# Optimization experiments

Measured on AMD Instinct MI355X. Metric: run time of the kernel, lower is better.

The kernel has to match this reference:

```python
import jax, jax.numpy as jnp
import numpy as np

N_NODES = 100000
N_HEDGES = 20000
N_PAIRS = 1600000
D = 128


def setup_inputs() -> dict:
    key = jax.random.key(0)
    k1, k2, k3, k4, k5 = jax.random.split(key, 5)
    features = jax.random.normal(k1, (N_NODES, D), dtype=jnp.float32)
    W = jax.random.normal(k2, (D, D), dtype=jnp.float32) * (1.0 / np.sqrt(D))
    b = jax.random.normal(k3, (D,), dtype=jnp.float32) * 0.01
    node_idx = jax.random.randint(k4, (N_PAIRS,), 0, N_NODES, dtype=jnp.int32)
    hedge_idx = jax.random.randint(k5, (N_PAIRS,), 0, N_HEDGES, dtype=jnp.int32)
    return {"features": features, "W": W, "b": b,
            "node_idx": node_idx, "hedge_idx": hedge_idx, "n_hedges": N_HEDGES}


def reference(features, W, b, node_idx, hedge_idx, n_hedges):
    # features: [N, D]; (node_idx, hedge_idx): [E] incidence pairs
    N = features.shape[0]
    ones = jnp.ones(node_idx.shape, dtype=features.dtype)
    # node -> hyperedge mean (DGL copy_u + mean over 'in' etype)
    deg_e = jax.ops.segment_sum(ones, hedge_idx, num_segments=n_hedges)  # [He]
    h_edge = jax.ops.segment_sum(features[node_idx], hedge_idx, num_segments=n_hedges)
    h_edge = h_edge / jnp.maximum(deg_e, 1.0)[:, None]  # zero-degree edges -> 0
    # hyperedge -> node mean (copy_u + mean over 'contains' etype)
    deg_n = jax.ops.segment_sum(ones, node_idx, num_segments=N)  # [N]
    h_node = jax.ops.segment_sum(h_edge[hedge_idx], node_idx, num_segments=N)
    h_node = h_node / jnp.maximum(deg_n, 1.0)[:, None]
    # nn.Linear: x @ W.T + b
    return h_node @ W.T + b
```

## Files before the change

kernel.cpp:

```cpp
#include <hip/hip_runtime.h>

static constexpr int kD = 128;
static constexpr int kHedges = 20000;

static constexpr int kNCE = 157;
static constexpr int kCapCE = 11264;
static constexpr int kNCN = 196;
static constexpr int kCapCN = 9216;
static constexpr int kSliceE4 = 1664;
static constexpr int kSliceN4 = 1408;
static constexpr int kPmax = 3200;

__device__ __forceinline__ float u2f(unsigned u) { return __uint_as_float(u); }
__device__ __forceinline__ unsigned f2u(float f) { return __float_as_uint(f); }

__device__ __forceinline__ unsigned bfpack(float x, float y) {
  unsigned ux = f2u(x); ux = (ux + 0x7FFFu + ((ux >> 16) & 1u)) >> 16;
  unsigned uy = f2u(y); uy = (uy + 0x7FFFu + ((uy >> 16) & 1u)) & 0xFFFF0000u;
  return ux | uy;
}
__device__ __forceinline__ void bf8_acc(uint4 v, float* a) {
  a[0] += u2f(v.x << 16); a[1] += u2f(v.x & 0xFFFF0000u);
  a[2] += u2f(v.y << 16); a[3] += u2f(v.y & 0xFFFF0000u);
  a[4] += u2f(v.z << 16); a[5] += u2f(v.z & 0xFFFF0000u);
  a[6] += u2f(v.w << 16); a[7] += u2f(v.w & 0xFFFF0000u);
}

__global__ __launch_bounds__(256) void partition_coarse(
    const float* __restrict__ feat, unsigned* __restrict__ feat_bf, int n_feat,
    const int* __restrict__ node_idx, const int* __restrict__ hedge_idx,
    int n_pairs,
    int* __restrict__ gcnt_e, int* __restrict__ buf_e,
    int* __restrict__ gcnt_n, int* __restrict__ buf_n) {
  __shared__ unsigned lbuf_e[kPmax];
  __shared__ unsigned lbuf_n[kPmax];
  __shared__ int he[kNCE], se[kNCE];
  __shared__ int hn[kNCN], sn_[kNCN];
  __shared__ int wtot[4];
  const int tid = threadIdx.x;
  {
    const int n8 = n_feat >> 3;
    for (int t = blockIdx.x * 256 + tid; t < n8; t += gridDim.x * 256) {
      long long i = (long long)t * 8;
      const float4 v0 = *(const float4*)(feat + i);
      const float4 v1 = *(const float4*)(feat + i + 4);
      uint4 o;
      o.x = bfpack(v0.x, v0.y); o.y = bfpack(v0.z, v0.w);
      o.z = bfpack(v1.x, v1.y); o.w = bfpack(v1.z, v1.w);
      *(uint4*)(feat_bf + (i >> 1)) = o;
    }
  }
  const int per_block = (n_pairs + gridDim.x - 1) / gridDim.x;
  const int s = blockIdx.x * per_block;
  const int e = min(s + per_block, n_pairs);
  const int cnt = max(e - s, 0);
  for (int i = tid; i < kNCE; i += 256) he[i] = 0;
  for (int i = tid; i < kNCN; i += 256) hn[i] = 0;
  __syncthreads();
  for (int i = s + tid; i < e; i += 256) {
    atomicAdd(&he[hedge_idx[i] >> 7], 1);
    atomicAdd(&hn[node_idx[i] >> 9], 1);
  }
  __syncthreads();
  const int lane = tid & 63, wid = tid >> 6;
  {
    int v = (tid < kNCE) ? he[tid] : 0;
    int x = v;
#pragma unroll
    for (int d = 1; d < 64; d <<= 1) {
      int y = __shfl_up(x, d, 64);
      if (lane >= d) x += y;
    }
    if (lane == 63) wtot[wid] = x;
    __syncthreads();
    int add = 0;
    for (int w = 0; w < wid; ++w) add += wtot[w];
    if (tid < kNCE) {
      int lofs = x + add - v;
      int base = (v > 0) ? atomicAdd(&gcnt_e[tid], v) : 0;
      se[tid] = base - lofs;
      he[tid] = lofs;
    }
  }
  __syncthreads();
  {
    int v = (tid < kNCN) ? hn[tid] : 0;
    int x = v;
#pragma unroll
    for (int d = 1; d < 64; d <<= 1) {
      int y = __shfl_up(x, d, 64);
      if (lane >= d) x += y;
    }
    if (lane == 63) wtot[wid] = x;
    __syncthreads();
    int add = 0;
    for (int w = 0; w < wid; ++w) add += wtot[w];
    if (tid < kNCN) {
      int lofs = x + add - v;
      int base = (v > 0) ? atomicAdd(&gcnt_n[tid], v) : 0;
      sn_[tid] = base - lofs;
      hn[tid] = lofs;
    }
  }
  __syncthreads();
  for (int i = s + tid; i < e; i += 256) {
    const unsigned n = (unsigned)node_idx[i];
    const unsigned h = (unsigned)hedge_idx[i];
    const int be = (int)(h >> 7);
    const int p = atomicAdd(&he[be], 1);
    lbuf_e[p] = (n << 15) | h;
    const int bn = (int)(n >> 9);
    const int q = atomicAdd(&hn[bn], 1);
    lbuf_n[q] = (h << 17) | n;
  }
  __syncthreads();
  for (int i = tid; i < cnt; i += 256) {
    const unsigned v = lbuf_e[i];
    const int h = (int)(v & 0x7FFFu);
    const int n = (int)(v >> 15);
    const int b = h >> 7;
    const int pe = se[b] + i;
    if (pe < kCapCE) buf_e[(long long)b * kCapCE + pe] = (n << 7) | (h & 127);
  }
  for (int i = tid; i < cnt; i += 256) {
    const unsigned v = lbuf_n[i];
    const int n = (int)(v & 0x1FFFFu);
    const int h = (int)(v >> 17);
    const int b = n >> 9;
    const int pn = sn_[b] + i;
    if (pn < kCapCN) buf_n[(long long)b * kCapCN + pn] = (h << 9) | (n & 511);
  }
}

__global__ __launch_bounds__(512) void subsort_kernel(
    int* __restrict__ buf_e, const int* __restrict__ gcnt_e, int* __restrict__ seg_e,
    int* __restrict__ buf_n, const int* __restrict__ gcnt_n, int* __restrict__ seg_n) {
  __shared__ int sbuf[kCapCE];
  __shared__ int bins[513];
  __shared__ int cur[512];
  __shared__ int segs[513];
  __shared__ int wtot[8];
  const int tid = threadIdx.x;
  int nbins, shift, cnt; int* src; int* segout;
  if (blockIdx.x < kNCE) {
    int cb = blockIdx.x; nbins = 128; shift = 7;
    src = buf_e + (long long)cb * kCapCE;
    cnt = min(gcnt_e[cb], kCapCE);
    segout = seg_e + cb * 129;
  } else {
    int cb = blockIdx.x - kNCE; nbins = 512; shift = 9;
    src = buf_n + (long long)cb * kCapCN;
    cnt = min(gcnt_n[cb], kCapCN);
    segout = seg_n + cb * 513;
  }
  const int mask = nbins - 1;
  for (int i = tid; i < nbins; i += 512) bins[i] = 0;
  __syncthreads();
  for (int i = tid; i < cnt; i += 512) atomicAdd(&bins[src[i] & mask], 1);
  __syncthreads();
  const int lane = tid & 63, wid = tid >> 6;
  int v = (tid < nbins) ? bins[tid] : 0;
  int x = v;
#pragma unroll
  for (int d = 1; d < 64; d <<= 1) {
    int y = __shfl_up(x, d, 64);
    if (lane >= d) x += y;
  }
  if (lane == 63) wtot[wid] = x;
  __syncthreads();
  int add = 0;
  for (int w = 0; w < wid; ++w) add += wtot[w];
  if (tid < nbins) { segs[tid + 1] = x + add; cur[tid] = x + add - v; }
  if (tid == 0) segs[0] = 0;
  __syncthreads();
  for (int i = tid; i < cnt; i += 512) {
    int p = src[i];
    int r = atomicAdd(&cur[p & mask], 1);
    sbuf[r] = p >> shift;
  }
  __syncthreads();
  for (int i = tid; i < cnt; i += 512) src[i] = sbuf[i];
  for (int j = tid; j <= nbins; j += 512) segout[j] = segs[j];
}

__global__ __launch_bounds__(256) void gather_edge_v4(
    const unsigned* __restrict__ feat_bf, const int* __restrict__ buf_e,
    const int* __restrict__ seg_e, unsigned* __restrict__ h_edge, int n_hedges) {
  __shared__ int ebuf[kSliceE4];
  __shared__ int segl[17];
  const int b = blockIdx.x;
  const int tid = threadIdx.x;
  const int h0 = b * 16;
  const int cb = h0 >> 7, j0 = h0 & 127;
  if (tid < 17) segl[tid] = seg_e[cb * 129 + j0 + tid];
  __syncthreads();
  const int sbase = segl[0];
  const int n_sl = min(segl[16] - sbase, kSliceE4);
  const int* src = buf_e + (long long)cb * kCapCE + sbase;
  for (int i = tid; i < n_sl; i += 256) ebuf[i] = src[i];
  __syncthreads();
  const int g = tid >> 4, lane = tid & 15, cw = lane * 4;
  int gh = h0 + g;
  if (gh >= n_hedges) return;
  const int deg = segl[g + 1] - segl[g];
  const int s0 = min(segl[g] - sbase, n_sl);
  const int e0 = min(segl[g + 1] - sbase, n_sl);
  float a[8] = {}, a2[8] = {};
  int j = s0;
  const int jend8 = s0 + ((e0 - s0) & ~7);
  if (j < jend8) {
    uint4 A0 = *(const uint4*)(feat_bf + (long long)ebuf[j] * 64 + cw);
    uint4 A1 = *(const uint4*)(feat_bf + (long long)ebuf[j + 1] * 64 + cw);
    uint4 A2 = *(const uint4*)(feat_bf + (long long)ebuf[j + 2] * 64 + cw);
    uint4 A3 = *(const uint4*)(feat_bf + (long long)ebuf[j + 3] * 64 + cw);
    uint4 A4 = *(const uint4*)(feat_bf + (long long)ebuf[j + 4] * 64 + cw);
    uint4 A5 = *(const uint4*)(feat_bf + (long long)ebuf[j + 5] * 64 + cw);
    uint4 A6 = *(const uint4*)(feat_bf + (long long)ebuf[j + 6] * 64 + cw);
    uint4 A7 = *(const uint4*)(feat_bf + (long long)ebuf[j + 7] * 64 + cw);
    j += 8;
    for (; j < jend8; j += 8) {
      uint4 B0 = *(const uint4*)(feat_bf + (long long)ebuf[j] * 64 + cw);
      uint4 B1 = *(const uint4*)(feat_bf + (long long)ebuf[j + 1] * 64 + cw);
      uint4 B2 = *(const uint4*)(feat_bf + (long long)ebuf[j + 2] * 64 + cw);
      uint4 B3 = *(const uint4*)(feat_bf + (long long)ebuf[j + 3] * 64 + cw);
      uint4 B4 = *(const uint4*)(feat_bf + (long long)ebuf[j + 4] * 64 + cw);
      uint4 B5 = *(const uint4*)(feat_bf + (long long)ebuf[j + 5] * 64 + cw);
      uint4 B6 = *(const uint4*)(feat_bf + (long long)ebuf[j + 6] * 64 + cw);
      uint4 B7 = *(const uint4*)(feat_bf + (long long)ebuf[j + 7] * 64 + cw);
      bf8_acc(A0, a); bf8_acc(A1, a2); bf8_acc(A2, a); bf8_acc(A3, a2);
      bf8_acc(A4, a); bf8_acc(A5, a2); bf8_acc(A6, a); bf8_acc(A7, a2);
      A0 = B0; A1 = B1; A2 = B2; A3 = B3;
      A4 = B4; A5 = B5; A6 = B6; A7 = B7;
    }
    bf8_acc(A0, a); bf8_acc(A1, a2); bf8_acc(A2, a); bf8_acc(A3, a2);
    bf8_acc(A4, a); bf8_acc(A5, a2); bf8_acc(A6, a); bf8_acc(A7, a2);
  }
  for (; j < e0; ++j) {
    uint4 v = *(const uint4*)(feat_bf + (long long)ebuf[j] * 64 + cw);
    bf8_acc(v, a);
  }
#pragma unroll
  for (int t = 0; t < 8; ++t) a[t] += a2[t];
  float inv = 1.0f / fmaxf((float)deg, 1.0f);
  uint4 o;
  o.x = bfpack(a[0] * inv, a[1] * inv);
  o.y = bfpack(a[2] * inv, a[3] * inv);
  o.z = bfpack(a[4] * inv, a[5] * inv);
  o.w = bfpack(a[6] * inv, a[7] * inv);
  *(uint4*)(h_edge + (long long)gh * 64 + cw) = o;
}

static constexpr int kWRow = 68;
__global__ __launch_bounds__(256) void edge_linear_v4(
    unsigned* __restrict__ h_edge, const float* __restrict__ W, int n_rows) {
  __shared__ unsigned Wt2[kD * kWRow];
  __shared__ float hT[kD * 64];
  const int tid = threadIdx.x;
  const int row0 = blockIdx.x * 64;
  for (int i = tid; i < kD * 64; i += 256) {
    int k = i & 127, j = i >> 7;
    float c0 = W[(2 * j) * kD + k];
    float c1 = W[(2 * j + 1) * kD + k];
    Wt2[k * kWRow + j] = bfpack(c0, c1);
  }
  {
    const int r = tid & 63, o = tid >> 6;
    const uint4* hp = (const uint4*)(h_edge + (long long)(row0 + r) * 64 + o * 16);
#pragma unroll
    for (int q = 0; q < 4; ++q) {
      uint4 v = hp[q];
      int k0 = o * 32 + q * 8;
      hT[(k0 + 0) * 64 + r] = u2f(v.x << 16);
      hT[(k0 + 1) * 64 + r] = u2f(v.x & 0xFFFF0000u);
      hT[(k0 + 2) * 64 + r] = u2f(v.y << 16);
      hT[(k0 + 3) * 64 + r] = u2f(v.y & 0xFFFF0000u);
      hT[(k0 + 4) * 64 + r] = u2f(v.z << 16);
      hT[(k0 + 5) * 64 + r] = u2f(v.z & 0xFFFF0000u);
      hT[(k0 + 6) * 64 + r] = u2f(v.w << 16);
      hT[(k0 + 7) * 64 + r] = u2f(v.w & 0xFFFF0000u);
    }
  }
  __syncthreads();
  const int c8 = tid & 15;
  const int rg = tid >> 4;
  float4 acc[4][2] = {};
#pragma unroll 2
  for (int k = 0; k < kD; ++k) {
    const uint4 wp = *(const uint4*)(&Wt2[k * kWRow + c8 * 4]);
    const float4 h4 = *(const float4*)(&hT[k * 64 + rg * 4]);
    const float w0 = u2f(wp.x << 16), w1 = u2f(wp.x & 0xFFFF0000u);
    const float w2 = u2f(wp.y << 16), w3 = u2f(wp.y & 0xFFFF0000u);
    const float w4 = u2f(wp.z << 16), w5 = u2f(wp.z & 0xFFFF0000u);
    const float w6 = u2f(wp.w << 16), w7 = u2f(wp.w & 0xFFFF0000u);
    const float hh[4] = {h4.x, h4.y, h4.z, h4.w};
#pragma unroll
    for (int i = 0; i < 4; ++i) {
      acc[i][0].x = fmaf(hh[i], w0, acc[i][0].x);
      acc[i][0].y = fmaf(hh[i], w1, acc[i][0].y);
      acc[i][0].z = fmaf(hh[i], w2, acc[i][0].z);
      acc[i][0].w = fmaf(hh[i], w3, acc[i][0].w);
      acc[i][1].x = fmaf(hh[i], w4, acc[i][1].x);
      acc[i][1].y = fmaf(hh[i], w5, acc[i][1].y);
      acc[i][1].z = fmaf(hh[i], w6, acc[i][1].z);
      acc[i][1].w = fmaf(hh[i], w7, acc[i][1].w);
    }
  }
  long long rr = row0 + rg * 4;
#pragma unroll
  for (int i = 0; i < 4; ++i) {
    uint4 o;
    o.x = bfpack(acc[i][0].x, acc[i][0].y);
    o.y = bfpack(acc[i][0].z, acc[i][0].w);
    o.z = bfpack(acc[i][1].x, acc[i][1].y);
    o.w = bfpack(acc[i][1].z, acc[i][1].w);
    *(uint4*)(h_edge + (rr + i) * 64 + c8 * 4) = o;
  }
}

__global__ __launch_bounds__(256) void gather_node_v4(
    const unsigned* __restrict__ t_edge, const int* __restrict__ buf_n,
    const int* __restrict__ seg_n, const float* __restrict__ bias,
    float* __restrict__ out, int n_nodes) {
  __shared__ int ebuf[kSliceN4];
  __shared__ int segl[65];
  const int b = blockIdx.x;
  const int tid = threadIdx.x;
  const int n0 = b * 64;
  const int cb = n0 >> 9, j0 = n0 & 511;
  if (tid < 65) segl[tid] = seg_n[cb * 513 + j0 + tid];
  __syncthreads();
  const int sbase = segl[0];
  const int n_sl = min(segl[64] - sbase, kSliceN4);
  const int* src = buf_n + (long long)cb * kCapCN + sbase;
  for (int i = tid; i < n_sl; i += 256) ebuf[i] = src[i];
  __syncthreads();
  const int g = tid >> 4, lane = tid & 15, cw = lane * 4;
  const float4 b0 = *(const float4*)(bias + lane * 8);
  const float4 b1 = *(const float4*)(bias + lane * 8 + 4);
  for (int nl = g; nl < 64; nl += 16) {
    int gn = n0 + nl;
    if (gn >= n_nodes) continue;
    const int deg = segl[nl + 1] - segl[nl];
    const int s0 = min(segl[nl] - sbase, n_sl);
    const int e0 = min(segl[nl + 1] - sbase, n_sl);
    float a[8] = {}, a2[8] = {};
    int j = s0;
    const int jend8 = s0 + ((e0 - s0) & ~7);
    if (j < jend8) {
      uint4 A0 = *(const uint4*)(t_edge + (long long)ebuf[j] * 64 + cw);
      uint4 A1 = *(const uint4*)(t_edge + (long long)ebuf[j + 1] * 64 + cw);
      uint4 A2 = *(const uint4*)(t_edge + (long long)ebuf[j + 2] * 64 + cw);
      uint4 A3 = *(const uint4*)(t_edge + (long long)ebuf[j + 3] * 64 + cw);
      uint4 A4 = *(const uint4*)(t_edge + (long long)ebuf[j + 4] * 64 + cw);
      uint4 A5 = *(const uint4*)(t_edge + (long long)ebuf[j + 5] * 64 + cw);
      uint4 A6 = *(const uint4*)(t_edge + (long long)ebuf[j + 6] * 64 + cw);
      uint4 A7 = *(const uint4*)(t_edge + (long long)ebuf[j + 7] * 64 + cw);
      j += 8;
      for (; j < jend8; j += 8) {
        uint4 B0 = *(const uint4*)(t_edge + (long long)ebuf[j] * 64 + cw);
        uint4 B1 = *(const uint4*)(t_edge + (long long)ebuf[j + 1] * 64 + cw);
        uint4 B2 = *(const uint4*)(t_edge + (long long)ebuf[j + 2] * 64 + cw);
        uint4 B3 = *(const uint4*)(t_edge + (long long)ebuf[j + 3] * 64 + cw);
        uint4 B4 = *(const uint4*)(t_edge + (long long)ebuf[j + 4] * 64 + cw);
        uint4 B5 = *(const uint4*)(t_edge + (long long)ebuf[j + 5] * 64 + cw);
        uint4 B6 = *(const uint4*)(t_edge + (long long)ebuf[j + 6] * 64 + cw);
        uint4 B7 = *(const uint4*)(t_edge + (long long)ebuf[j + 7] * 64 + cw);
        bf8_acc(A0, a); bf8_acc(A1, a2); bf8_acc(A2, a); bf8_acc(A3, a2);
        bf8_acc(A4, a); bf8_acc(A5, a2); bf8_acc(A6, a); bf8_acc(A7, a2);
        A0 = B0; A1 = B1; A2 = B2; A3 = B3;
        A4 = B4; A5 = B5; A6 = B6; A7 = B7;
      }
      bf8_acc(A0, a); bf8_acc(A1, a2); bf8_acc(A2, a); bf8_acc(A3, a2);
      bf8_acc(A4, a); bf8_acc(A5, a2); bf8_acc(A6, a); bf8_acc(A7, a2);
    }
    for (; j < e0; ++j) {
      uint4 v = *(const uint4*)(t_edge + (long long)ebuf[j] * 64 + cw);
      bf8_acc(v, a);
    }
#pragma unroll
    for (int t = 0; t < 8; ++t) a[t] += a2[t];
    float inv = 1.0f / fmaxf((float)deg, 1.0f);
    float4 o0, o1;
    o0.x = fmaf(a[0], inv, b0.x); o0.y = fmaf(a[1], inv, b0.y);
    o0.z = fmaf(a[2], inv, b0.z); o0.w = fmaf(a[3], inv, b0.w);
    o1.x = fmaf(a[4], inv, b1.x); o1.y = fmaf(a[5], inv, b1.y);
    o1.z = fmaf(a[6], inv, b1.z); o1.w = fmaf(a[7], inv, b1.w);
    float* op = out + (long long)gn * kD + lane * 8;
    *(float4*)op = o0;
    *(float4*)(op + 4) = o1;
  }
}

extern "C" void kernel_launch(void* const* d_in, const int* in_sizes, int n_in,
                              void* d_out, int out_size, void* d_ws, size_t ws_size,
                              hipStream_t stream) {
  const float* feat      = (const float*)d_in[0];
  const float* W         = (const float*)d_in[1];
  const float* b         = (const float*)d_in[2];
  const int*   node_idx  = (const int*)d_in[3];
  const int*   hedge_idx = (const int*)d_in[4];

  const int n_pairs  = in_sizes[3];
  const int n_nodes  = in_sizes[0] / kD;
  const int n_hedges = kHedges;
  const int n_feat   = in_sizes[0];

  unsigned* feat_bf = (unsigned*)d_out;

  const int n_rows_pad = ((n_hedges + 63) / 64) * 64;
  unsigned* h_edge = (unsigned*)d_ws;
  int* buf_e = (int*)(h_edge + (size_t)n_rows_pad * 64);
  int* buf_n = buf_e + (size_t)kNCE * kCapCE;
  int* seg_e = buf_n + (size_t)kNCN * kCapCN;
  int* seg_n = seg_e + (size_t)kNCE * 129;
  int* gcnt_e = seg_n + (size_t)kNCN * 513;
  int* gcnt_n = gcnt_e + kNCE;

  hipMemsetAsync(gcnt_e, 0, (size_t)(kNCE + kNCN) * sizeof(int), stream);

  int pgrid = (n_pairs + kPmax - 1) / kPmax;
  if (pgrid < 512) pgrid = 512;

  partition_coarse<<<pgrid, 256, 0, stream>>>(
      feat, feat_bf, n_feat,
      node_idx, hedge_idx, n_pairs, gcnt_e, buf_e, gcnt_n, buf_n);

  subsort_kernel<<<kNCE + kNCN, 512, 0, stream>>>(
      buf_e, gcnt_e, seg_e, buf_n, gcnt_n, seg_n);

  gather_edge_v4<<<(n_hedges + 15) / 16, 256, 0, stream>>>(
      feat_bf, buf_e, seg_e, h_edge, n_hedges);

  edge_linear_v4<<<n_rows_pad / 64, 256, 0, stream>>>(h_edge, W, n_rows_pad);

  gather_node_v4<<<(n_nodes + 63) / 64, 256, 0, stream>>>(
      h_edge, buf_n, seg_n, b, (float*)d_out, n_nodes);
}
```

Baseline: 278.9 us.

## Fuse edge linear transform into edge gather and widen subsort blocks

Merges the hyperedge mean-gather and the per-edge linear projection into one kernel. Each block keeps its 16 averaged rows in shared memory and multiplies them by a bf16 copy of W, so the intermediate h_edge round trip and one launch go away. The cost is that every one of the 1250 blocks now rebuilds the transposed W in shared memory, which adds about 34KB of LDS per block and could cut occupancy in the gather phase. Separately, the subsort kernel now runs with 1024 threads per block instead of 512.

```diff
diff --git a/kernel.cpp b/kernel.cpp
--- a/kernel.cpp
+++ b/kernel.cpp
@@ -10,6 +10,7 @@
 static constexpr int kSliceE4 = 1664;
 static constexpr int kSliceN4 = 1408;
 static constexpr int kPmax = 3200;
+static constexpr int kWRow = 68;
 
 __device__ __forceinline__ float u2f(unsigned u) { return __uint_as_float(u); }
 __device__ __forceinline__ unsigned f2u(float f) { return __float_as_uint(f); }
@@ -132,14 +133,14 @@
   }
 }
 
-__global__ __launch_bounds__(512) void subsort_kernel(
+__global__ __launch_bounds__(1024) void subsort_kernel(
     int* __restrict__ buf_e, const int* __restrict__ gcnt_e, int* __restrict__ seg_e,
     int* __restrict__ buf_n, const int* __restrict__ gcnt_n, int* __restrict__ seg_n) {
   __shared__ int sbuf[kCapCE];
   __shared__ int bins[513];
   __shared__ int cur[512];
   __shared__ int segs[513];
-  __shared__ int wtot[8];
+  __shared__ int wtot[16];
   const int tid = threadIdx.x;
   int nbins, shift, cnt; int* src; int* segout;
   if (blockIdx.x < kNCE) {
@@ -154,9 +155,9 @@
     segout = seg_n + cb * 513;
   }
   const int mask = nbins - 1;
-  for (int i = tid; i < nbins; i += 512) bins[i] = 0;
-  __syncthreads();
-  for (int i = tid; i < cnt; i += 512) atomicAdd(&bins[src[i] & mask], 1);
+  for (int i = tid; i < nbins; i += 1024) bins[i] = 0;
+  __syncthreads();
+  for (int i = tid; i < cnt; i += 1024) atomicAdd(&bins[src[i] & mask], 1);
   __syncthreads();
   const int lane = tid & 63, wid = tid >> 6;
   int v = (tid < nbins) ? bins[tid] : 0;
@@ -173,147 +174,115 @@
   if (tid < nbins) { segs[tid + 1] = x + add; cur[tid] = x + add - v; }
   if (tid == 0) segs[0] = 0;
   __syncthreads();
-  for (int i = tid; i < cnt; i += 512) {
+  for (int i = tid; i < cnt; i += 1024) {
     int p = src[i];
     int r = atomicAdd(&cur[p & mask], 1);
     sbuf[r] = p >> shift;
   }
   __syncthreads();
-  for (int i = tid; i < cnt; i += 512) src[i] = sbuf[i];
-  for (int j = tid; j <= nbins; j += 512) segout[j] = segs[j];
-}
-
-__global__ __launch_bounds__(256) void gather_edge_v4(
+  for (int i = tid; i < cnt; i += 1024) src[i] = sbuf[i];
+  for (int j = tid; j <= nbins; j += 1024) segout[j] = segs[j];
+}
+
+__global__ __launch_bounds__(256) void gather_edge_fused(
     const unsigned* __restrict__ feat_bf, const int* __restrict__ buf_e,
-    const int* __restrict__ seg_e, unsigned* __restrict__ h_edge, int n_hedges) {
+    const int* __restrict__ seg_e, const float* __restrict__ W,
+    unsigned* __restrict__ t_edge, int n_hedges) {
   __shared__ int ebuf[kSliceE4];
   __shared__ int segl[17];
+  __shared__ unsigned Wt2[kD * kWRow];
+  __shared__ float hrow[16][132];
   const int b = blockIdx.x;
   const int tid = threadIdx.x;
   const int h0 = b * 16;
   const int cb = h0 >> 7, j0 = h0 & 127;
   if (tid < 17) segl[tid] = seg_e[cb * 129 + j0 + tid];
-  __syncthreads();
-  const int sbase = segl[0];
-  const int n_sl = min(segl[16] - sbase, kSliceE4);
-  const int* src = buf_e + (long long)cb * kCapCE + sbase;
-  for (int i = tid; i < n_sl; i += 256) ebuf[i] = src[i];
-  __syncthreads();
-  const int g = tid >> 4, lane = tid & 15, cw = lane * 4;
-  int gh = h0 + g;
-  if (gh >= n_hedges) return;
-  const int deg = segl[g + 1] - segl[g];
-  const int s0 = min(segl[g] - sbase, n_sl);
-  const int e0 = min(segl[g + 1] - sbase, n_sl);
-  float a[8] = {}, a2[8] = {};
-  int j = s0;
-  const int jend8 = s0 + ((e0 - s0) & ~7);
-  if (j < jend8) {
-    uint4 A0 = *(const uint4*)(feat_bf + (long long)ebuf[j] * 64 + cw);
-    uint4 A1 = *(const uint4*)(feat_bf + (long long)ebuf[j + 1] * 64 + cw);
-    uint4 A2 = *(const uint4*)(feat_bf + (long long)ebuf[j + 2] * 64 + cw);
-    uint4 A3 = *(const uint4*)(feat_bf + (long long)ebuf[j + 3] * 64 + cw);
-    uint4 A4 = *(const uint4*)(feat_bf + (long long)ebuf[j + 4] * 64 + cw);
-    uint4 A5 = *(const uint4*)(feat_bf + (long long)ebuf[j + 5] * 64 + cw);
-    uint4 A6 = *(const uint4*)(feat_bf + (long long)ebuf[j + 6] * 64 + cw);
-    uint4 A7 = *(const uint4*)(feat_bf + (long long)ebuf[j + 7] * 64 + cw);
-    j += 8;
-    for (; j < jend8; j += 8) {
-      uint4 B0 = *(const uint4*)(feat_bf + (long long)ebuf[j] * 64 + cw);
-      uint4 B1 = *(const uint4*)(feat_bf + (long long)ebuf[j + 1] * 64 + cw);
-      uint4 B2 = *(const uint4*)(feat_bf + (long long)ebuf[j + 2] * 64 + cw);
-      uint4 B3 = *(const uint4*)(feat_bf + (long long)ebuf[j + 3] * 64 + cw);
-      uint4 B4 = *(const uint4*)(feat_bf + (long long)ebuf[j + 4] * 64 + cw);
-      uint4 B5 = *(const uint4*)(feat_bf + (long long)ebuf[j + 5] * 64 + cw);
-      uint4 B6 = *(const uint4*)(feat_bf + (long long)ebuf[j + 6] * 64 + cw);
-      uint4 B7 = *(const uint4*)(feat_bf + (long long)ebuf[j + 7] * 64 + cw);
-      bf8_acc(A0, a); bf8_acc(A1, a2); bf8_acc(A2, a); bf8_acc(A3, a2);
-      bf8_acc(A4, a); bf8_acc(A5, a2); bf8_acc(A6, a); bf8_acc(A7, a2);
-      A0 = B0; A1 = B1; A2 = B2; A3 = B3;
-      A4 = B4; A5 = B5; A6 = B6; A7 = B7;
-    }
-    bf8_acc(A0, a); bf8_acc(A1, a2); bf8_acc(A2, a); bf8_acc(A3, a2);
-    bf8_acc(A4, a); bf8_acc(A5, a2); bf8_acc(A6, a); bf8_acc(A7, a2);
-  }
-  for (; j < e0; ++j) {
-    uint4 v = *(const uint4*)(feat_bf + (long long)ebuf[j] * 64 + cw);
-    bf8_acc(v, a);
-  }
-#pragma unroll
-  for (int t = 0; t < 8; ++t) a[t] += a2[t];
-  float inv = 1.0f / fmaxf((float)deg, 1.0f);
-  uint4 o;
-  o.x = bfpack(a[0] * inv, a[1] * inv);
-  o.y = bfpack(a[2] * inv, a[3] * inv);
-  o.z = bfpack(a[4] * inv, a[5] * inv);
-  o.w = bfpack(a[6] * inv, a[7] * inv);
-  *(uint4*)(h_edge + (long long)gh * 64 + cw) = o;
-}
-
-static constexpr int kWRow = 68;
-__global__ __launch_bounds__(256) void edge_linear_v4(
-    unsigned* __restrict__ h_edge, const float* __restrict__ W, int n_rows) {
-  __shared__ unsigned Wt2[kD * kWRow];
-  __shared__ float hT[kD * 64];
-  const int tid = threadIdx.x;
-  const int row0 = blockIdx.x * 64;
   for (int i = tid; i < kD * 64; i += 256) {
     int k = i & 127, j = i >> 7;
     float c0 = W[(2 * j) * kD + k];
     float c1 = W[(2 * j + 1) * kD + k];
     Wt2[k * kWRow + j] = bfpack(c0, c1);
   }
+  __syncthreads();
+  const int sbase = segl[0];
+  const int n_sl = min(segl[16] - sbase, kSliceE4);
+  const int* src = buf_e + (long long)cb * kCapCE + sbase;
+  for (int i = tid; i < n_sl; i += 256) ebuf[i] = src[i];
+  __syncthreads();
+  const int g = tid >> 4, lane = tid & 15, cw = lane * 4;
+  const int gh = h0 + g;
+  float a[8] = {}, a2[8] = {};
+  int deg = 0;
+  if (gh < n_hedges) {
+    deg = segl[g + 1] - segl[g];
+    const int s0 = min(segl[g] - sbase, n_sl);
+    const int e0 = min(segl[g + 1] - sbase, n_sl);
+    int j = s0;
+    const int jend8 = s0 + ((e0 - s0) & ~7);
+    if (j < jend8) {
+      uint4 A0 = *(const uint4*)(feat_bf + (long long)ebuf[j] * 64 + cw);
+      uint4 A1 = *(const uint4*)(feat_bf + (long long)ebuf[j + 1] * 64 + cw);
+      uint4 A2 = *(const uint4*)(feat_bf + (long long)ebuf[j + 2] * 64 + cw);
+      uint4 A3 = *(const uint4*)(feat_bf + (long long)ebuf[j + 3] * 64 + cw);
+      uint4 A4 = *(const uint4*)(feat_bf + (long long)ebuf[j + 4] * 64 + cw);
+      uint4 A5 = *(const uint4*)(feat_bf + (long long)ebuf[j + 5] * 64 + cw);
+      uint4 A6 = *(const uint4*)(feat_bf + (long long)ebuf[j + 6] * 64 + cw);
+      uint4 A7 = *(const uint4*)(feat_bf + (long long)ebuf[j + 7] * 64 + cw);
+      j += 8;
+      for (; j < jend8; j += 8) {
+        uint4 B0 = *(const uint4*)(feat_bf + (long long)ebuf[j] * 64 + cw);
+        uint4 B1 = *(const uint4*)(feat_bf + (long long)ebuf[j + 1] * 64 + cw);
+        uint4 B2 = *(const uint4*)(feat_bf + (long long)ebuf[j + 2] * 64 + cw);
+        uint4 B3 = *(const uint4*)(feat_bf + (long long)ebuf[j + 3] * 64 + cw);
+        uint4 B4 = *(const uint4*)(feat_bf + (long long)ebuf[j + 4] * 64 + cw);
+        uint4 B5 = *(const uint4*)(feat_bf + (long long)ebuf[j + 5] * 64 + cw);
+        uint4 B6 = *(const uint4*)(feat_bf + (long long)ebuf[j + 6] * 64 + cw);
+        uint4 B7 = *(const uint4*)(feat_bf + (long long)ebuf[j + 7] * 64 + cw);
+        bf8_acc(A0, a); bf8_acc(A1, a2); bf8_acc(A2, a); bf8_acc(A3, a2);
+        bf8_acc(A4, a); bf8_acc(A5, a2); bf8_acc(A6, a); bf8_acc(A7, a2);
+        A0 = B0; A1 = B1; A2 = B2; A3 = B3;
+        A4 = B4; A5 = B5; A6 = B6; A7 = B7;
+      }
+      bf8_acc(A0, a); bf8_acc(A1, a2); bf8_acc(A2, a); bf8_acc(A3, a2);
+      bf8_acc(A4, a); bf8_acc(A5, a2); bf8_acc(A6, a); bf8_acc(A7, a2);
+    }
+    for (; j < e0; ++j) {
+      uint4 v = *(const uint4*)(feat_bf + (long long)ebuf[j] * 64 + cw);
+      bf8_acc(v, a);
+    }
+  }
   {
-    const int r = tid & 63, o = tid >> 6;
-    const uint4* hp = (const uint4*)(h_edge + (long long)(row0 + r) * 64 + o * 16);
-#pragma unroll
-    for (int q = 0; q < 4; ++q) {
-      uint4 v = hp[q];
-      int k0 = o * 32 + q * 8;
-      hT[(k0 + 0) * 64 + r] = u2f(v.x << 16);
-      hT[(k0 + 1) * 64 + r] = u2f(v.x & 0xFFFF0000u);
-      hT[(k0 + 2) * 64 + r] = u2f(v.y << 16);
-      hT[(k0 + 3) * 64 + r] = u2f(v.y & 0xFFFF0000u);
-      hT[(k0 + 4) * 64 + r] = u2f(v.z << 16);
-      hT[(k0 + 5) * 64 + r] = u2f(v.z & 0xFFFF0000u);
-      hT[(k0 + 6) * 64 + r] = u2f(v.w << 16);
-      hT[(k0 + 7) * 64 + r] = u2f(v.w & 0xFFFF0000u);
-    }
-  }
-  __syncthreads();
-  const int c8 = tid & 15;
-  const int rg = tid >> 4;
-  float4 acc[4][2] = {};
+    const float inv = 1.0f / fmaxf((float)deg, 1.0f);
+    float4 r0, r1;
+    r0.x = (a[0] + a2[0]) * inv; r0.y = (a[1] + a2[1]) * inv;
+    r0.z = (a[2] + a2[2]) * inv; r0.w = (a[3] + a2[3]) * inv;
+    r1.x = (a[4] + a2[4]) * inv; r1.y = (a[5] + a2[5]) * inv;
+    r1.z = (a[6] + a2[6]) * inv; r1.w = (a[7] + a2[7]) * inv;
+    *(float4*)(&hrow[g][lane * 8]) = r0;
+    *(float4*)(&hrow[g][lane * 8 + 4]) = r1;
+  }
+  __syncthreads();
+  float acc[8] = {};
 #pragma unroll 2
   for (int k = 0; k < kD; ++k) {
-    const uint4 wp = *(const uint4*)(&Wt2[k * kWRow + c8 * 4]);
-    const float4 h4 = *(const float4*)(&hT[k * 64 + rg * 4]);
-    const float w0 = u2f(wp.x << 16), w1 = u2f(wp.x & 0xFFFF0000u);
-    const float w2 = u2f(wp.y << 16), w3 = u2f(wp.y & 0xFFFF0000u);
-    const float w4 = u2f(wp.z << 16), w5 = u2f(wp.z & 0xFFFF0000u);
-    const float w6 = u2f(wp.w << 16), w7 = u2f(wp.w & 0xFFFF0000u);
-    const float hh[4] = {h4.x, h4.y, h4.z, h4.w};
-#pragma unroll
-    for (int i = 0; i < 4; ++i) {
-      acc[i][0].x = fmaf(hh[i], w0, acc[i][0].x);
-      acc[i][0].y = fmaf(hh[i], w1, acc[i][0].y);
-      acc[i][0].z = fmaf(hh[i], w2, acc[i][0].z);
-      acc[i][0].w = fmaf(hh[i], w3, acc[i][0].w);
-      acc[i][1].x = fmaf(hh[i], w4, acc[i][1].x);
-      acc[i][1].y = fmaf(hh[i], w5, acc[i][1].y);
-      acc[i][1].z = fmaf(hh[i], w6, acc[i][1].z);
-      acc[i][1].w = fmaf(hh[i], w7, acc[i][1].w);
-    }
-  }
-  long long rr = row0 + rg * 4;
-#pragma unroll
-  for (int i = 0; i < 4; ++i) {
+    const uint4 wp = *(const uint4*)(&Wt2[k * kWRow + lane * 4]);
+    const float hk = hrow[g][k];
+    acc[0] = fmaf(hk, u2f(wp.x << 16), acc[0]);
+    acc[1] = fmaf(hk, u2f(wp.x & 0xFFFF0000u), acc[1]);
+    acc[2] = fmaf(hk, u2f(wp.y << 16), acc[2]);
+    acc[3] = fmaf(hk, u2f(wp.y & 0xFFFF0000u), acc[3]);
+    acc[4] = fmaf(hk, u2f(wp.z << 16), acc[4]);
+    acc[5] = fmaf(hk, u2f(wp.z & 0xFFFF0000u), acc[5]);
+    acc[6] = fmaf(hk, u2f(wp.w << 16), acc[6]);
+    acc[7] = fmaf(hk, u2f(wp.w & 0xFFFF0000u), acc[7]);
+  }
+  if (gh < n_hedges) {
     uint4 o;
-    o.x = bfpack(acc[i][0].x, acc[i][0].y);
-    o.y = bfpack(acc[i][0].z, acc[i][0].w);
-    o.z = bfpack(acc[i][1].x, acc[i][1].y);
-    o.w = bfpack(acc[i][1].z, acc[i][1].w);
-    *(uint4*)(h_edge + (rr + i) * 64 + c8 * 4) = o;
+    o.x = bfpack(acc[0], acc[1]);
+    o.y = bfpack(acc[2], acc[3]);
+    o.z = bfpack(acc[4], acc[5]);
+    o.w = bfpack(acc[6], acc[7]);
+    *(uint4*)(t_edge + (long long)gh * 64 + cw) = o;
   }
 }
 
@@ -408,8 +377,8 @@
   unsigned* feat_bf = (unsigned*)d_out;
 
   const int n_rows_pad = ((n_hedges + 63) / 64) * 64;
-  unsigned* h_edge = (unsigned*)d_ws;
-  int* buf_e = (int*)(h_edge + (size_t)n_rows_pad * 64);
+  unsigned* t_edge = (unsigned*)d_ws;
+  int* buf_e = (int*)(t_edge + (size_t)n_rows_pad * 64);
   int* buf_n = buf_e + (size_t)kNCE * kCapCE;
   int* seg_e = buf_n + (size_t)kNCN * kCapCN;
   int* seg_n = seg_e + (size_t)kNCE * 129;
@@ -425,14 +394,12 @@
       feat, feat_bf, n_feat,
       node_idx, hedge_idx, n_pairs, gcnt_e, buf_e, gcnt_n, buf_n);
 
-  subsort_kernel<<<kNCE + kNCN, 512, 0, stream>>>(
+  subsort_kernel<<<kNCE + kNCN, 1024, 0, stream>>>(
       buf_e, gcnt_e, seg_e, buf_n, gcnt_n, seg_n);
 
-  gather_edge_v4<<<(n_hedges + 15) / 16, 256, 0, stream>>>(
-      feat_bf, buf_e, seg_e, h_edge, n_hedges);
-
-  edge_linear_v4<<<n_rows_pad / 64, 256, 0, stream>>>(h_edge, W, n_rows_pad);
+  gather_edge_fused<<<(n_hedges + 15) / 16, 256, 0, stream>>>(
+      feat_bf, buf_e, seg_e, W, t_edge, n_hedges);
 
   gather_node_v4<<<(n_nodes + 63) / 64, 256, 0, stream>>>(
-      h_edge, buf_n, seg_n, b, (float*)d_out, n_nodes);
-}
+      t_edge, buf_n, seg_n, b, (float*)d_out, n_nodes);
+}
```

Measured after the change: 276.5 us. About the same (-0.9%).
